# Kernel tuning notes

Measured on AMD Instinct MI355X. Metric: run time of the kernel, lower is better.

The kernel has to match this reference:

```python
import jax, jax.numpy as jnp
import numpy as np

WIDTH = 1024
HEADS = 16
INIT_SCALE = 0.02


def setup_inputs() -> dict:
    key = jax.random.key(0)
    ks = jax.random.split(key, 5)
    x = jax.random.normal(ks[0], (2, 2048, WIDTH), dtype=jnp.float32)
    # torch Linear weight [out, in]; we store transposed [in, out] for x @ W
    W_qkv = jax.random.normal(ks[1], (WIDTH, 3 * WIDTH), dtype=jnp.float32) * INIT_SCALE
    b_qkv = jnp.zeros((3 * WIDTH,), dtype=jnp.float32)
    W_proj = jax.random.normal(ks[2], (WIDTH, WIDTH), dtype=jnp.float32) * INIT_SCALE
    b_proj = jnp.zeros((WIDTH,), dtype=jnp.float32)
    return {"x": x, "W_qkv": W_qkv, "b_qkv": b_qkv, "W_proj": W_proj, "b_proj": b_proj}


def reference(x, W_qkv, b_qkv, W_proj, b_proj):
    bs, n_ctx, width = x.shape
    heads = HEADS
    attn_ch = width // heads  # per-head channel dim (width*3 // heads // 3)
    scale = 1.0 / np.sqrt(np.sqrt(attn_ch))  # applied to both q and k

    qkv = x @ W_qkv + b_qkv                      # [b, t, 3*width]
    qkv = qkv.reshape(bs, n_ctx, heads, 3 * attn_ch)
    q, k, v = jnp.split(qkv, 3, axis=-1)         # each [b, t, h, c]

    weight = jnp.einsum('bthc,bshc->bhts', q * scale, k * scale)
    wdtype = weight.dtype
    weight = jax.nn.softmax(weight.astype(jnp.float32), axis=-1).astype(wdtype)

    out = jnp.einsum('bhts,bshc->bthc', weight, v).reshape(bs, n_ctx, width)
    return out @ W_proj + b_proj
```

## Files before the change

### kernel.cpp

```cpp
#include <hip/hip_runtime.h>

typedef __attribute__((ext_vector_type(4))) float fx4;
typedef __attribute__((ext_vector_type(16))) float f32x16;
typedef __attribute__((ext_vector_type(8))) short s16x8;
typedef __attribute__((ext_vector_type(2))) unsigned int u32x2;

#define QK_SCALE 0.35355339059327373f
#define LOG2E    1.4426950408889634f

__device__ __forceinline__ short f2bf(float f) {
  union { float f; unsigned int u; } v; v.f = f;
  unsigned int r = v.u + 0x7fffu + ((v.u >> 16) & 1u);
  return (short)(r >> 16);
}

__device__ __forceinline__ unsigned f2u(float f) {
  union { float f; unsigned u; } v; v.f = f; return v.u;
}
__device__ __forceinline__ float u2f(unsigned u) {
  union { unsigned u; float f; } v; v.u = u; return v.f;
}
__device__ __forceinline__ float bf2f(short s) {
  return u2f(((unsigned)(unsigned short)s) << 16);
}

__device__ __forceinline__ float xhalf_sum(float x) {
  u32x2 r = __builtin_amdgcn_permlane32_swap(f2u(x), f2u(x), false, false);
  return u2f(r[0]) + u2f(r[1]);
}

__device__ __forceinline__ int swz(int row, int cb) {
  return (row * 128 + cb) ^ ((row & 7) << 4);
}

#define GLL(g, lds) __builtin_amdgcn_global_load_lds( \
    (__attribute__((address_space(1))) void*)(void*)(g), \
    (__attribute__((address_space(3))) void*)(void*)(lds), 16, 0, 0)

__global__ __launch_bounds__(256) void prep(
    const float* __restrict__ x, short* __restrict__ x16,
    const float* __restrict__ Wqkv, short* __restrict__ WqkvT,
    const float* __restrict__ Wproj, short* __restrict__ WprojT) {
  const int b = blockIdx.x;
  if (b < 4096) {
    int i = b * 256 + threadIdx.x;
    float4 v = reinterpret_cast<const float4*>(x)[i];
    short4 o;
    o.x = f2bf(v.x); o.y = f2bf(v.y); o.z = f2bf(v.z); o.w = f2bf(v.w);
    reinterpret_cast<short4*>(x16)[i] = o;
    return;
  }
  __shared__ float tile[32][33];
  const float* W; short* WT; int N, bx, by;
  if (b < 7168) { W = Wqkv; WT = WqkvT; N = 3072; int r = b - 4096; bx = r % 96; by = r / 96; }
  else          { W = Wproj; WT = WprojT; N = 1024; int r = b - 7168; bx = r % 32; by = r / 32; }
  const int K = 1024;
  int tx = threadIdx.x & 31, ty = threadIdx.x >> 5;
  int n0 = bx * 32, k0 = by * 32;
#pragma unroll
  for (int i = 0; i < 32; i += 8)
    tile[ty + i][tx] = W[(size_t)(k0 + ty + i) * N + n0 + tx];
  __syncthreads();
#pragma unroll
  for (int i = 0; i < 32; i += 8)
    WT[(size_t)(n0 + ty + i) * K + k0 + tx] = f2bf(tile[tx][ty + i]);
}

template <int MODE, int BK, int BN>
__global__ __launch_bounds__(BN * 4, 4) void gemm_bf16(
    const short* __restrict__ A, const short* __restrict__ Bt,
    const float* __restrict__ bias, float* __restrict__ Cout,
    short* __restrict__ Qo, short* __restrict__ Ko, short* __restrict__ Vo,
    int M, int N, int K) {
  constexpr int T = BN * 4;
  constexpr int NWC = BN / 32;
  constexpr int CA = 16 * BK / T;
  constexpr int CB = BK / 32;
  __shared__ __align__(16) char sA[2][128 * BK * 2];
  __shared__ __align__(16) char sB[2][BN * BK * 2];
  const int tid = threadIdx.x;
  const int w = tid >> 6, l = tid & 63;
  const int lr = l & 15, lg = l >> 4;
  const int bid = blockIdx.x;
  const int m0 = ((bid & 7) * 4 + ((bid >> 3) & 3)) * 128;
  const int n0 = (bid >> 5) * BN;
  const int wr = (w / NWC) * 64, wc = (w % NWC) * 32;

  fx4 accT[2][4] = {};

  auto stage = [&](int kt, int buf) {
#pragma unroll
    for (int i = 0; i < CA; ++i) {
      int c = i * T + tid;
      int r, lch;
      if (BK == 64) { r = c >> 3; lch = (c & 7) ^ (r & 7); }
      else          { r = c >> 2; lch = (c & 3) ^ (r & 3); }
      GLL(A + (size_t)(m0 + r) * K + kt + lch * 8, sA[buf] + c * 16);
    }
#pragma unroll
    for (int i = 0; i < CB; ++i) {
      int c = i * T + tid;
      int r, lch;
      if (BK == 64) { r = c >> 3; lch = (c & 7) ^ (r & 7); }
      else          { r = c >> 2; lch = (c & 3) ^ (r & 3); }
      GLL(Bt + (size_t)(n0 + r) * K + kt + lch * 8, sB[buf] + c * 16);
    }
  };
  auto roff = [&](int R, int kk) {
    return (BK == 64) ? ((R * 128 + kk * 64 + lg * 16) ^ ((R & 7) << 4))
                      : ((R * 64 + lg * 16) ^ ((R & 3) << 4));
  };

  stage(0, 0);
  __syncthreads();

  const int NIT = K / BK;
  int cur = 0;
  for (int it = 0; it < NIT; ++it) {
    if (it + 1 < NIT) stage((it + 1) * BK, cur ^ 1);
#pragma unroll
    for (int kk = 0; kk < (BK == 64 ? 2 : 1); ++kk) {
      s16x8 av[4], bv[2];
#pragma unroll
      for (int m = 0; m < 4; ++m)
        av[m] = *reinterpret_cast<const s16x8*>(sA[cur] + roff(wr + m * 16 + lr, kk));
#pragma unroll
      for (int n = 0; n < 2; ++n)
        bv[n] = *reinterpret_cast<const s16x8*>(sB[cur] + roff(wc + n * 16 + lr, kk));
#pragma unroll
      for (int n = 0; n < 2; ++n)
#pragma unroll
        for (int m = 0; m < 4; ++m)
          accT[n][m] = __builtin_amdgcn_mfma_f32_16x16x32_bf16(bv[n], av[m], accT[n][m], 0, 0, 0);
    }
    __syncthreads();
    cur ^= 1;
  }

#pragma unroll
  for (int n = 0; n < 2; ++n) {
    const int col0 = n0 + wc + n * 16 + lg * 4;
    const float4 bs = *reinterpret_cast<const float4*>(bias + col0);
    if (MODE == 1) {
#pragma unroll
      for (int m = 0; m < 4; ++m) {
        int row = m0 + wr + m * 16 + lr;
        float4 v;
        v.x = accT[n][m][0] + bs.x; v.y = accT[n][m][1] + bs.y;
        v.z = accT[n][m][2] + bs.z; v.w = accT[n][m][3] + bs.w;
        *reinterpret_cast<float4*>(Cout + (size_t)row * N + col0) = v;
      }
    } else {
      const int h = col0 / 192;
      const int rr = col0 - h * 192;
#pragma unroll
      for (int m = 0; m < 4; ++m) {
        int row = m0 + wr + m * 16 + lr;
        int b = row >> 11, t = row & 2047;
        size_t bh = (size_t)b * 16 + h;
        float v0 = accT[n][m][0] + bs.x, v1 = accT[n][m][1] + bs.y;
        float v2 = accT[n][m][2] + bs.z, v3 = accT[n][m][3] + bs.w;
        if (rr < 64) {
          short4 s4;
          s4.x = f2bf(v0 * (QK_SCALE * LOG2E)); s4.y = f2bf(v1 * (QK_SCALE * LOG2E));
          s4.z = f2bf(v2 * (QK_SCALE * LOG2E)); s4.w = f2bf(v3 * (QK_SCALE * LOG2E));
          *reinterpret_cast<short4*>(Qo + (bh * 2048 + t) * 64 + rr) = s4;
        } else if (rr < 128) {
          short4 s4;
          s4.x = f2bf(v0 * QK_SCALE); s4.y = f2bf(v1 * QK_SCALE);
          s4.z = f2bf(v2 * QK_SCALE); s4.w = f2bf(v3 * QK_SCALE);
          *reinterpret_cast<short4*>(Ko + (bh * 2048 + t) * 64 + (rr - 64)) = s4;
        } else {
          Vo[(bh * 64 + (rr - 128) + 0) * 2048 + t] = f2bf(v0);
          Vo[(bh * 64 + (rr - 128) + 1) * 2048 + t] = f2bf(v1);
          Vo[(bh * 64 + (rr - 128) + 2) * 2048 + t] = f2bf(v2);
          Vo[(bh * 64 + (rr - 128) + 3) * 2048 + t] = f2bf(v3);
        }
      }
    }
  }
}

__global__ __launch_bounds__(256, 4) void attn_fwd(
    const short* __restrict__ Q, const short* __restrict__ Kc,
    const short* __restrict__ VT, short* __restrict__ OW,
    float* __restrict__ ML) {
  __shared__ __align__(16) char sK[2][8192];
  __shared__ __align__(16) char sV[2][8192];
  const int tid = threadIdx.x;
  const int w = tid >> 6, l = tid & 63;
  const int l31 = l & 31, hi = l >> 5;
  const int bid = blockIdx.x;
  const int bh = (bid & 7) * 4 + ((bid >> 3) & 3);
  const int rest = bid >> 5;
  const int qt = rest >> 1, half = rest & 1;
  const int q0 = qt * 128 + w * 32;
  const int sbase = half * 1024;

  s16x8 qf[4];
  const short* qp = Q + ((size_t)bh * 2048 + q0 + l31) * 64 + hi * 8;
#pragma unroll
  for (int ks = 0; ks < 4; ++ks)
    qf[ks] = *reinterpret_cast<const s16x8*>(qp + ks * 16);

  float lsum = 0.f;
  f32x16 o0 = {}, o1 = {};

#pragma unroll
  for (int i = 0; i < 2; ++i) {
    int c = i * 256 + tid, r = c >> 3, pch = c & 7, lch = pch ^ (r & 7);
    GLL(Kc + ((size_t)bh * 2048 + sbase + r) * 64 + lch * 8, sK[0] + c * 16);
    GLL(VT + ((size_t)bh * 64 + r) * 2048 + sbase + lch * 8, sV[0] + c * 16);
  }
  __syncthreads();

  for (int sb = 0; sb < 16; ++sb) {
    const int s0 = sbase + sb * 64;
    if (sb < 15) {
#pragma unroll
      for (int i = 0; i < 2; ++i) {
        int c = i * 256 + tid, r = c >> 3, pch = c & 7, lch = pch ^ (r & 7);
        GLL(Kc + ((size_t)bh * 2048 + s0 + 64 + r) * 64 + lch * 8, sK[(sb + 1) & 1] + c * 16);
        GLL(VT + ((size_t)bh * 64 + r) * 2048 + s0 + 64 + lch * 8, sV[(sb + 1) & 1] + c * 16);
      }
    }
    const char* kb = sK[sb & 1];
    const char* vb = sV[sb & 1];

    f32x16 p0 = {}, p1 = {};
    __builtin_amdgcn_s_setprio(1);
#pragma unroll
    for (int ks = 0; ks < 4; ++ks) {
      int off = swz(l31, ks * 32 + hi * 16);
      s16x8 ka0 = *reinterpret_cast<const s16x8*>(kb + off);
      s16x8 ka1 = *reinterpret_cast<const s16x8*>(kb + off + 4096);
      p0 = __builtin_amdgcn_mfma_f32_32x32x16_bf16(ka0, qf[ks], p0, 0, 0, 0);
      p1 = __builtin_amdgcn_mfma_f32_32x32x16_bf16(ka1, qf[ks], p1, 0, 0, 0);
    }
    __builtin_amdgcn_s_setprio(0);

#pragma unroll
    for (int i = 0; i < 16; ++i) {
      p0[i] = __builtin_amdgcn_exp2f(p0[i]);
      p1[i] = __builtin_amdgcn_exp2f(p1[i]);
    }
    float s8[8];
#pragma unroll
    for (int i = 0; i < 8; ++i)
      s8[i] = (p0[2 * i] + p0[2 * i + 1]) + (p1[2 * i] + p1[2 * i + 1]);
    lsum += ((s8[0] + s8[1]) + (s8[2] + s8[3])) + ((s8[4] + s8[5]) + (s8[6] + s8[7]));

    int wd[16];
#pragma unroll
    for (int i = 0; i < 8; ++i) {
      asm("v_cvt_pk_bf16_f32 %0, %1, %2" : "=v"(wd[i]) : "v"(p0[2 * i]), "v"(p0[2 * i + 1]));
      asm("v_cvt_pk_bf16_f32 %0, %1, %2" : "=v"(wd[8 + i]) : "v"(p1[2 * i]), "v"(p1[2 * i + 1]));
    }

    __builtin_amdgcn_s_setprio(1);
#pragma unroll
    for (int t = 0; t < 4; ++t) {
      u32x2 s02 = __builtin_amdgcn_permlane32_swap(
          (unsigned)wd[4 * t], (unsigned)wd[4 * t + 2], false, false);
      u32x2 s13 = __builtin_amdgcn_permlane32_swap(
          (unsigned)wd[4 * t + 1], (unsigned)wd[4 * t + 3], false, false);
      union { unsigned i4[4]; s16x8 v; } fr;
      fr.i4[0] = s02[0]; fr.i4[1] = s13[0]; fr.i4[2] = s02[1]; fr.i4[3] = s13[1];
      int off = swz(l31, t * 32 + hi * 16);
      s16x8 v0 = *reinterpret_cast<const s16x8*>(vb + off);
      s16x8 v1 = *reinterpret_cast<const s16x8*>(vb + off + 4096);
      o0 = __builtin_amdgcn_mfma_f32_32x32x16_bf16(v0, fr.v, o0, 0, 0, 0);
      o1 = __builtin_amdgcn_mfma_f32_32x32x16_bf16(v1, fr.v, o1, 0, 0, 0);
    }
    __builtin_amdgcn_s_setprio(0);
    __syncthreads();
  }

  short* owp = OW + (((size_t)(half * 32 + bh) * 2048) + q0 + l31) * 64 + hi * 4;
#pragma unroll
  for (int gq = 0; gq < 4; ++gq) {
    short4 s4;
    s4.x = f2bf(o0[4 * gq]);     s4.y = f2bf(o0[4 * gq + 1]);
    s4.z = f2bf(o0[4 * gq + 2]); s4.w = f2bf(o0[4 * gq + 3]);
    *reinterpret_cast<short4*>(owp + 8 * gq) = s4;
    s4.x = f2bf(o1[4 * gq]);     s4.y = f2bf(o1[4 * gq + 1]);
    s4.z = f2bf(o1[4 * gq + 2]); s4.w = f2bf(o1[4 * gq + 3]);
    *reinterpret_cast<short4*>(owp + 32 + 8 * gq) = s4;
  }
  float lt = xhalf_sum(lsum);
  if (hi == 0)
    ML[(size_t)(half * 32 + bh) * 2048 + q0 + l31] = lt;
}

__global__ __launch_bounds__(256) void attn_merge(
    const short* __restrict__ OW, const float* __restrict__ ML,
    short* __restrict__ Y) {
  int gid = blockIdx.x * 256 + threadIdx.x;
  int row = gid >> 3, dc = (gid & 7) * 8;
  float inv = 1.f / (ML[row] + ML[65536 + row]);
  s16x8 a = *reinterpret_cast<const s16x8*>(OW + (size_t)row * 64 + dc);
  s16x8 bb = *reinterpret_cast<const s16x8*>(OW + (size_t)65536 * 64 + (size_t)row * 64 + dc);
  int bh = row >> 11, q = row & 2047;
  int b = bh >> 4, h = bh & 15;
  short* yp = Y + ((size_t)b * 2048 + q) * 1024 + h * 64 + dc;
  s16x8 o;
#pragma unroll
  for (int i = 0; i < 8; ++i)
    o[i] = f2bf((bf2f(a[i]) + bf2f(bb[i])) * inv);
  *reinterpret_cast<s16x8*>(yp) = o;
}

extern "C" void kernel_launch(void* const* d_in, const int* in_sizes, int n_in,
                              void* d_out, int out_size, void* d_ws, size_t ws_size,
                              hipStream_t stream) {
  const float* x     = (const float*)d_in[0];
  const float* Wqkv  = (const float*)d_in[1];
  const float* bqkv  = (const float*)d_in[2];
  const float* Wproj = (const float*)d_in[3];
  const float* bproj = (const float*)d_in[4];
  float* out = (float*)d_out;

  char* ws = (char*)d_ws;
  const size_t MB = 1024 * 1024;
  short* x16    = (short*)(ws);
  short* WqkvT  = (short*)(ws + 8 * MB);
  short* WprojT = (short*)(ws + 14 * MB);
  short* Q16    = (short*)(ws + 16 * MB);
  short* K16    = (short*)(ws + 24 * MB);
  short* VT16   = (short*)(ws + 32 * MB);
  short* OW     = (short*)(ws + 40 * MB);
  float* ML     = (float*)(ws + 58 * MB);
  short* Y16    = x16;

  prep<<<8192, 256, 0, stream>>>(x, x16, Wqkv, WqkvT, Wproj, WprojT);
  gemm_bf16<0, 32, 128><<<768, 512, 0, stream>>>(x16, WqkvT, bqkv, nullptr,
                                                 Q16, K16, VT16, 4096, 3072, 1024);
  attn_fwd<<<1024, 256, 0, stream>>>(Q16, K16, VT16, OW, ML);
  attn_merge<<<2048, 256, 0, stream>>>(OW, ML, Y16);
  gemm_bf16<1, 64, 64><<<512, 256, 0, stream>>>(Y16, WprojT, bproj, out,
                                                nullptr, nullptr, nullptr, 4096, 1024, 1024);
}
```

Before: 116.8 us.

## Fuse split-KV attention halves into one 512-thread block, merge in LDS

The two key halves of each query tile now run as two groups of four waves inside one 512-thread block instead of two separate blocks. At the end, the second group writes its partial output and row sums to shared memory, and the first group combines them, normalizes and writes the final bf16 output directly. This removes the separate merge kernel, one launch, and the global round trip of the partial outputs and sums. In exchange the block uses 64KB of LDS and twice the threads, which may lower occupancy and adds a block-wide barrier before the epilogue.

New measurement: 110.1 us, median of 2. 1.06x faster.

```diff
diff --git a/kernel.cpp b/kernel.cpp
--- a/kernel.cpp
+++ b/kernel.cpp
@@ -19,9 +19,6 @@
 }
 __device__ __forceinline__ float u2f(unsigned u) {
   union { unsigned u; float f; } v; v.u = u; return v.f;
-}
-__device__ __forceinline__ float bf2f(short s) {
-  return u2f(((unsigned)(unsigned short)s) << 16);
 }
 
 __device__ __forceinline__ float xhalf_sum(float x) {
@@ -181,21 +178,25 @@
   }
 }
 
-__global__ __launch_bounds__(256, 4) void attn_fwd(
+__global__ __launch_bounds__(512, 4) void attn_fwd(
     const short* __restrict__ Q, const short* __restrict__ Kc,
-    const short* __restrict__ VT, short* __restrict__ OW,
-    float* __restrict__ ML) {
-  __shared__ __align__(16) char sK[2][8192];
-  __shared__ __align__(16) char sV[2][8192];
+    const short* __restrict__ VT, short* __restrict__ Y) {
+  __shared__ __align__(16) char smem[65536];
   const int tid = threadIdx.x;
-  const int w = tid >> 6, l = tid & 63;
+  const int w = tid >> 6;
+  const int wq = w & 3;
+  const int half = w >> 2;
+  const int t8 = tid & 255;
+  const int l = tid & 63;
   const int l31 = l & 31, hi = l >> 5;
   const int bid = blockIdx.x;
   const int bh = (bid & 7) * 4 + ((bid >> 3) & 3);
-  const int rest = bid >> 5;
-  const int qt = rest >> 1, half = rest & 1;
-  const int q0 = qt * 128 + w * 32;
+  const int qt = bid >> 5;
+  const int q0 = qt * 128 + wq * 32;
   const int sbase = half * 1024;
+
+  char* kbase = smem + half * 16384;
+  char* vbase = smem + 32768 + half * 16384;
 
   s16x8 qf[4];
   const short* qp = Q + ((size_t)bh * 2048 + q0 + l31) * 64 + hi * 8;
@@ -208,24 +209,26 @@
 
 #pragma unroll
   for (int i = 0; i < 2; ++i) {
-    int c = i * 256 + tid, r = c >> 3, pch = c & 7, lch = pch ^ (r & 7);
-    GLL(Kc + ((size_t)bh * 2048 + sbase + r) * 64 + lch * 8, sK[0] + c * 16);
-    GLL(VT + ((size_t)bh * 64 + r) * 2048 + sbase + lch * 8, sV[0] + c * 16);
+    int c = i * 256 + t8, r = c >> 3, pch = c & 7, lch = pch ^ (r & 7);
+    GLL(Kc + ((size_t)bh * 2048 + sbase + r) * 64 + lch * 8, kbase + c * 16);
+    GLL(VT + ((size_t)bh * 64 + r) * 2048 + sbase + lch * 8, vbase + c * 16);
   }
   __syncthreads();
 
   for (int sb = 0; sb < 16; ++sb) {
     const int s0 = sbase + sb * 64;
     if (sb < 15) {
+      char* kn = kbase + ((sb + 1) & 1) * 8192;
+      char* vn = vbase + ((sb + 1) & 1) * 8192;
 #pragma unroll
       for (int i = 0; i < 2; ++i) {
-        int c = i * 256 + tid, r = c >> 3, pch = c & 7, lch = pch ^ (r & 7);
-        GLL(Kc + ((size_t)bh * 2048 + s0 + 64 + r) * 64 + lch * 8, sK[(sb + 1) & 1] + c * 16);
-        GLL(VT + ((size_t)bh * 64 + r) * 2048 + s0 + 64 + lch * 8, sV[(sb + 1) & 1] + c * 16);
+        int c = i * 256 + t8, r = c >> 3, pch = c & 7, lch = pch ^ (r & 7);
+        GLL(Kc + ((size_t)bh * 2048 + s0 + 64 + r) * 64 + lch * 8, kn + c * 16);
+        GLL(VT + ((size_t)bh * 64 + r) * 2048 + s0 + 64 + lch * 8, vn + c * 16);
       }
     }
-    const char* kb = sK[sb & 1];
-    const char* vb = sV[sb & 1];
+    const char* kb = kbase + (sb & 1) * 8192;
+    const char* vb = vbase + (sb & 1) * 8192;
 
     f32x16 p0 = {}, p1 = {};
     __builtin_amdgcn_s_setprio(1);
@@ -276,38 +279,41 @@
     __syncthreads();
   }
 
-  short* owp = OW + (((size_t)(half * 32 + bh) * 2048) + q0 + l31) * 64 + hi * 4;
-#pragma unroll
-  for (int gq = 0; gq < 4; ++gq) {
-    short4 s4;
-    s4.x = f2bf(o0[4 * gq]);     s4.y = f2bf(o0[4 * gq + 1]);
-    s4.z = f2bf(o0[4 * gq + 2]); s4.w = f2bf(o0[4 * gq + 3]);
-    *reinterpret_cast<short4*>(owp + 8 * gq) = s4;
-    s4.x = f2bf(o1[4 * gq]);     s4.y = f2bf(o1[4 * gq + 1]);
-    s4.z = f2bf(o1[4 * gq + 2]); s4.w = f2bf(o1[4 * gq + 3]);
-    *reinterpret_cast<short4*>(owp + 32 + 8 * gq) = s4;
-  }
   float lt = xhalf_sum(lsum);
-  if (hi == 0)
-    ML[(size_t)(half * 32 + bh) * 2048 + q0 + l31] = lt;
-}
-
-__global__ __launch_bounds__(256) void attn_merge(
-    const short* __restrict__ OW, const float* __restrict__ ML,
-    short* __restrict__ Y) {
-  int gid = blockIdx.x * 256 + threadIdx.x;
-  int row = gid >> 3, dc = (gid & 7) * 8;
-  float inv = 1.f / (ML[row] + ML[65536 + row]);
-  s16x8 a = *reinterpret_cast<const s16x8*>(OW + (size_t)row * 64 + dc);
-  s16x8 bb = *reinterpret_cast<const s16x8*>(OW + (size_t)65536 * 64 + (size_t)row * 64 + dc);
-  int bh = row >> 11, q = row & 2047;
-  int b = bh >> 4, h = bh & 15;
-  short* yp = Y + ((size_t)b * 2048 + q) * 1024 + h * 64 + dc;
-  s16x8 o;
-#pragma unroll
-  for (int i = 0; i < 8; ++i)
-    o[i] = f2bf((bf2f(a[i]) + bf2f(bb[i])) * inv);
-  *reinterpret_cast<s16x8*>(yp) = o;
+  float* scr = (float*)smem;
+  float* slsum = (float*)(smem + 32768);
+  if (half == 1) {
+    float* op = scr + wq * 2048;
+#pragma unroll
+    for (int gq = 0; gq < 4; ++gq)
+#pragma unroll
+      for (int j = 0; j < 4; ++j) {
+        op[(hi * 4 + 8 * gq + j) * 32 + l31] = o0[4 * gq + j];
+        op[(32 + hi * 4 + 8 * gq + j) * 32 + l31] = o1[4 * gq + j];
+      }
+    if (hi == 0) slsum[wq * 32 + l31] = lt;
+  }
+  __syncthreads();
+  if (half == 0) {
+    const int b = bh >> 4, h = bh & 15;
+    float inv = 1.f / (lt + slsum[wq * 32 + l31]);
+    const float* op = scr + wq * 2048;
+    short* yp = Y + ((size_t)b * 2048 + q0 + l31) * 1024 + h * 64 + hi * 4;
+#pragma unroll
+    for (int gq = 0; gq < 4; ++gq) {
+      short4 s4;
+      s4.x = f2bf((o0[4 * gq + 0] + op[(hi * 4 + 8 * gq + 0) * 32 + l31]) * inv);
+      s4.y = f2bf((o0[4 * gq + 1] + op[(hi * 4 + 8 * gq + 1) * 32 + l31]) * inv);
+      s4.z = f2bf((o0[4 * gq + 2] + op[(hi * 4 + 8 * gq + 2) * 32 + l31]) * inv);
+      s4.w = f2bf((o0[4 * gq + 3] + op[(hi * 4 + 8 * gq + 3) * 32 + l31]) * inv);
+      *reinterpret_cast<short4*>(yp + 8 * gq) = s4;
+      s4.x = f2bf((o1[4 * gq + 0] + op[(32 + hi * 4 + 8 * gq + 0) * 32 + l31]) * inv);
+      s4.y = f2bf((o1[4 * gq + 1] + op[(32 + hi * 4 + 8 * gq + 1) * 32 + l31]) * inv);
+      s4.z = f2bf((o1[4 * gq + 2] + op[(32 + hi * 4 + 8 * gq + 2) * 32 + l31]) * inv);
+      s4.w = f2bf((o1[4 * gq + 3] + op[(32 + hi * 4 + 8 * gq + 3) * 32 + l31]) * inv);
+      *reinterpret_cast<short4*>(yp + 32 + 8 * gq) = s4;
+    }
+  }
 }
 
 extern "C" void kernel_launch(void* const* d_in, const int* in_sizes, int n_in,
@@ -328,15 +334,12 @@
   short* Q16    = (short*)(ws + 16 * MB);
   short* K16    = (short*)(ws + 24 * MB);
   short* VT16   = (short*)(ws + 32 * MB);
-  short* OW     = (short*)(ws + 40 * MB);
-  float* ML     = (float*)(ws + 58 * MB);
   short* Y16    = x16;
 
   prep<<<8192, 256, 0, stream>>>(x, x16, Wqkv, WqkvT, Wproj, WprojT);
   gemm_bf16<0, 32, 128><<<768, 512, 0, stream>>>(x16, WqkvT, bqkv, nullptr,
                                                  Q16, K16, VT16, 4096, 3072, 1024);
-  attn_fwd<<<1024, 256, 0, stream>>>(Q16, K16, VT16, OW, ML);
-  attn_merge<<<2048, 256, 0, stream>>>(OW, ML, Y16);
+  attn_fwd<<<512, 512, 0, stream>>>(Q16, K16, VT16, Y16);
   gemm_bf16<1, 64, 64><<<512, 256, 0, stream>>>(Y16, WprojT, bproj, out,
                                                 nullptr, nullptr, nullptr, 4096, 1024, 1024);
 }
```
